# Optimization experiments

Hardware: AMD Instinct MI355X
Metric: run time of the kernel (lower is better)

## Reference

```python
import jax, jax.numpy as jnp
import numpy as np

N = 1048576        # batch
DTOT = 64          # total dims in u
D = 32             # transformed dims (len(nodes))
K = 40             # knots = num spline bins
B = 5.0            # tail bound: bins/2 = ceil(max|limit|)


def setup_inputs() -> dict:
    key = jax.random.key(0)
    k1, k2, k3, k4 = jax.random.split(key, 4)
    # scale inputs so they cover many bins and some fall in the identity tails
    u = jax.random.normal(k1, (N, DTOT), jnp.float32) * 3.0
    w = jax.random.uniform(k2, (D, K), jnp.float32, -0.5, 0.5)
    h = jax.random.uniform(k3, (D, K), jnp.float32, -0.5, 0.5)
    d = jax.random.uniform(k4, (D, K - 1), jnp.float32, -0.5, 0.5)
    nodes = jnp.arange(D, dtype=jnp.int32)
    return {"u": u, "w": w, "h": h, "d": d, "nodes": nodes}


def _rqs_forward(x, w, h, d):
    # x: [N, D] selected dims; w,h: [D, K]; d: [D, K-1]
    dt = x.dtype
    widths = jax.nn.softmax(w, axis=-1) * (2.0 * B)          # [D, K]
    cumw = jnp.concatenate(
        [jnp.full((D, 1), -B, dt), -B + jnp.cumsum(widths, -1)], -1)  # [D, K+1]
    heights = jax.nn.softmax(h, axis=-1) * (2.0 * B)
    cumh = jnp.concatenate(
        [jnp.full((D, 1), -B, dt), -B + jnp.cumsum(heights, -1)], -1)
    # interior derivatives via softplus, boundary derivatives fixed to 1 (linear tails)
    derivs = jnp.concatenate(
        [jnp.ones((D, 1), dt), jax.nn.softplus(d), jnp.ones((D, 1), dt)], -1)  # [D, K+1]

    inside = jnp.abs(x) <= B
    xc = jnp.clip(x, -B, B)
    # per-dim bin search (irregular, data-dependent)
    idx = jax.vmap(lambda kn, xd: jnp.searchsorted(kn, xd, side='right'))(cumw, xc.T).T - 1
    idx = jnp.clip(idx, 0, K - 1)                             # [N, D]

    dd = jnp.arange(D)[None, :]
    cw = cumw[dd, idx]; bw = widths[dd, idx]
    ch = cumh[dd, idx]; bh = heights[dd, idx]
    d0 = derivs[dd, idx]; d1 = derivs[dd, idx + 1]
    delta = bh / bw                                            # bin slope

    theta = (xc - cw) / bw
    t1m = theta * (1.0 - theta)
    denom = delta + (d0 + d1 - 2.0 * delta) * t1m
    num = bh * (delta * theta * theta + d0 * t1m)
    y = ch + num / denom
    logdet = (jnp.log(delta * delta * (d1 * theta * theta
                                       + 2.0 * delta * t1m
                                       + d0 * (1.0 - theta) ** 2))
              - 2.0 * jnp.log(denom))

    y = jnp.where(inside, y, x)                # identity tails
    logdet = jnp.where(inside, logdet, 0.0)
    return y, logdet.sum(-1)                   # [N, D], [N]


def reference(u, w, h, d, nodes):
    y, logd = _rqs_forward(u[:, nodes], w, h, d)
    x = u.at[:, nodes].set(y)
    return x, logd
```

## Files before the change

kernel.cpp:

```cpp
#include <hip/hip_runtime.h>
#include <math.h>

#define NROWS 1048576
#define DTOT  64
#define D     32
#define K     40
#define Bf    5.0f
#define G     128
#define GS    132
#define TP    (K + 1)

#define OFF_CUMW 0
#define OFF_DER  (D * (K + 1))
#define OFF_RBW  (2 * D * (K + 1))
#define OFF_CH   (2 * D * (K + 1) + D * K)
#define OFF_BH   (2 * D * (K + 1) + 2 * D * K)
#define OFF_GS_BYTES ((2 * D * (K + 1) + 3 * D * K) * 4)
#define WS_BYTES (OFF_GS_BYTES + D * G)

__global__ __launch_bounds__(64) void build_tables(
    const float* __restrict__ w, const float* __restrict__ h,
    const float* __restrict__ dk,
    float* __restrict__ cumw_g, float* __restrict__ der_g,
    float* __restrict__ rbw_g, float* __restrict__ ch_g,
    float* __restrict__ bh_g, unsigned char* __restrict__ gs_g)
{
    const int j = blockIdx.x;
    const int k = threadIdx.x;
    __shared__ float s_cumw[K + 1];

    float wv = (k < K) ? w[j * K + k] : -INFINITY;
    float hv = (k < K) ? h[j * K + k] : -INFINITY;
    float mw = wv, mh = hv;
    for (int m = 32; m > 0; m >>= 1) {
        mw = fmaxf(mw, __shfl_xor(mw, m));
        mh = fmaxf(mh, __shfl_xor(mh, m));
    }
    float ew = (k < K) ? __expf(wv - mw) : 0.f;
    float eh = (k < K) ? __expf(hv - mh) : 0.f;
    float sw = ew, sh = eh;
    for (int m = 32; m > 0; m >>= 1) {
        sw += __shfl_xor(sw, m);
        sh += __shfl_xor(sh, m);
    }
    float width  = ew / sw * (2.f * Bf);
    float height = eh / sh * (2.f * Bf);

    float iw = width, ih = height;
    for (int off = 1; off < 64; off <<= 1) {
        float a = __shfl_up(iw, off);
        float b = __shfl_up(ih, off);
        if (k >= off) { iw += a; ih += b; }
    }
    const float cw_k    = -Bf + (iw - width);
    const float ch_k    = -Bf + (ih - height);
    const float cw_next = -Bf + iw;

    if (k <= K) {
        float dv = 1.f;
        if (k > 0 && k < K) dv = log1pf(__expf(dk[j * (K - 1) + (k - 1)]));
        der_g[j * (K + 1) + k] = dv;
    }
    if (k < K) {
        cumw_g[j * (K + 1) + k] = cw_k;
        rbw_g[j * K + k] = 1.f / width;
        ch_g [j * K + k] = ch_k;
        bh_g [j * K + k] = height;
        s_cumw[k] = cw_k;
    }
    if (k == K - 1) {
        cumw_g[j * (K + 1) + K] = cw_next;
        s_cumw[K] = cw_next;
    }
    __syncthreads();

    for (int c = k; c < G; c += 64) {
        float L = -Bf + (2.f * Bf) * ((float)c / (float)G);
        int idx = 0;
        for (int m = 1; m < K; ++m)
            if (s_cumw[m] <= L) idx = m;
        gs_g[j * G + c] = (unsigned char)idx;
    }
}

__global__ __launch_bounds__(1024, 8) void rqs_main(
    const float4* __restrict__ u4,
    const float* __restrict__ cumw_g, const float* __restrict__ der_g,
    const float* __restrict__ rbw_g, const float* __restrict__ ch_g,
    const float* __restrict__ bh_g, const unsigned char* __restrict__ gs_g,
    float4* __restrict__ x4, float* __restrict__ logd, int ntiles)
{
    __shared__ float4 s_sel[D * TP];
    __shared__ float4 s_bin[D * TP];
    __shared__ unsigned char s_gs[D * GS];

    const int t = threadIdx.x;
    for (int e = t; e < D * K; e += 1024) {
        const int j = e / K, k = e - j * K;
        const float cw0 = cumw_g[j * (K + 1) + k];
        const float cw1 = cumw_g[j * (K + 1) + k + 1];
        const float rb0 = rbw_g[e];
        const float rb1 = (k < K - 1) ? rbw_g[e + 1] : 1.f;
        s_sel[j * TP + k] = make_float4(cw0, rb0, cw1, rb1);
        s_bin[j * TP + k] = make_float4(ch_g[e], bh_g[e],
                                        der_g[j * (K + 1) + k],
                                        der_g[j * (K + 1) + k + 1]);
    }
    for (int i = t; i < D * G / 4; i += 1024) {
        const int r = i >> 5, wi = i & 31;
        *(uint32_t*)(s_gs + r * GS + wi * 4) = ((const uint32_t*)gs_g)[i];
    }
    __syncthreads();

    const int seg = t & 7;
    const int rl  = t >> 3;

    int tile = blockIdx.x;
    float4 vt = make_float4(0.f, 0.f, 0.f, 0.f);
    float4 vp = make_float4(0.f, 0.f, 0.f, 0.f);
    if (tile < ntiles) {
        const int row = tile * 128 + rl;
        vt = u4[row * 16 + seg];
        vp = u4[row * 16 + 8 + seg];
    }

    for (; tile < ntiles; tile += gridDim.x) {
        const int next = tile + gridDim.x;
        float4 nt = make_float4(0.f, 0.f, 0.f, 0.f);
        float4 np = make_float4(0.f, 0.f, 0.f, 0.f);
        if (next < ntiles) {
            const int nrow = next * 128 + rl;
            nt = u4[nrow * 16 + seg];
            np = u4[nrow * 16 + 8 + seg];
        }

        const int row = tile * 128 + rl;
        x4[row * 16 + 8 + seg] = vp;

        float vv[4] = {vt.x, vt.y, vt.z, vt.w};
        float prod = 1.f;
#pragma unroll
        for (int c = 0; c < 4; ++c) {
            const int j = seg * 4 + c;
            const float x = vv[c];
            const bool inside = fabsf(x) <= Bf;
            const float xc = fminf(fmaxf(x, -Bf), Bf);

            int cell = (int)((xc + Bf) * (G / (2.f * Bf)));
            cell = min(cell, G - 1);
            int i = s_gs[j * GS + cell];

            const float4 s = s_sel[j * TP + i];
            const bool adv = (xc >= s.z) && (i < K - 1);
            const float cw  = adv ? s.z : s.x;
            const float rbw = adv ? s.w : s.y;
            i += adv;

            const float4 b = s_bin[j * TP + i];
            const float ch = b.x, bh = b.y, d0 = b.z, d1 = b.w;

            const float delta = bh * rbw;
            const float theta = (xc - cw) * rbw;
            const float omt   = 1.f - theta;
            const float t1m   = theta * omt;
            const float th2   = theta * theta;
            const float denom = fmaf(fmaf(-2.f, delta, d0 + d1), t1m, delta);
            const float num   = bh * fmaf(d0, t1m, delta * th2);
            const float rd    = __builtin_amdgcn_rcpf(denom);
            const float y     = fmaf(num, rd, ch);
            const float Ap    = fmaf(d1, th2,
                                 fmaf(2.f * delta, t1m, d0 * omt * omt));
            const float term  = delta * delta * Ap * (rd * rd);

            vv[c] = inside ? y : x;
            prod  = inside ? prod * term : prod;
        }
        x4[row * 16 + seg] = make_float4(vv[0], vv[1], vv[2], vv[3]);

        float ld = __logf(prod);
        ld += __shfl_xor(ld, 1);
        ld += __shfl_xor(ld, 2);
        ld += __shfl_xor(ld, 4);
        if (seg == 0) logd[row] = ld;

        vt = nt; vp = np;
    }
}

extern "C" void kernel_launch(void* const* d_in, const int* in_sizes, int n_in,
                              void* d_out, int out_size, void* d_ws, size_t ws_size,
                              hipStream_t stream) {
    const float* u  = (const float*)d_in[0];
    const float* w  = (const float*)d_in[1];
    const float* h  = (const float*)d_in[2];
    const float* dk = (const float*)d_in[3];

    float* ws   = (float*)d_ws;
    float* cumw = ws + OFF_CUMW;
    float* der  = ws + OFF_DER;
    float* rbw  = ws + OFF_RBW;
    float* ch   = ws + OFF_CH;
    float* bh   = ws + OFF_BH;
    unsigned char* gs = (unsigned char*)d_ws + OFF_GS_BYTES;

    float* xout = (float*)d_out;
    float* logd = (float*)d_out + (size_t)NROWS * DTOT;

    build_tables<<<D, 64, 0, stream>>>(w, h, dk, cumw, der, rbw, ch, bh, gs);

    const int ntiles = NROWS / 128;
    rqs_main<<<512, 1024, 0, stream>>>((const float4*)u, cumw, der, rbw, ch, bh,
                                       gs, (float4*)xout, logd, ntiles);
}
```

Baseline: 451.8 us.

## Use nontemporal stores, DPP reduction, and smaller blocks with a delayed passthrough load

Blocks shrink from 1024 to 512 threads and the grid grows from 512 to 768 blocks, so each tile now covers 64 rows. The passthrough half of each row is loaded in the current iteration instead of being prefetched, and both output halves plus logdet are written with nontemporal stores to reduce cache pollution. The 8-lane logdet reduction uses DPP row operations instead of shuffles. In exchange, loading the passthrough data late may expose its memory latency, and the DPP controls assume a fixed lane layout within each group of 8.

After: 465.8 us. 3.1% more time.

```diff
diff --git a/kernel.cpp b/kernel.cpp
--- a/kernel.cpp
+++ b/kernel.cpp
@@ -17,6 +17,18 @@
 #define OFF_BH   (2 * D * (K + 1) + 2 * D * K)
 #define OFF_GS_BYTES ((2 * D * (K + 1) + 3 * D * K) * 4)
 #define WS_BYTES (OFF_GS_BYTES + D * G)
+
+typedef float nt_f4 __attribute__((ext_vector_type(4)));
+
+__device__ __forceinline__ float dpp_add(float v, const int ctrl) {
+    int r;
+    switch (ctrl) {
+    case 0:  r = __builtin_amdgcn_update_dpp(0, __float_as_int(v), 0xB1,  0xF, 0xF, false); break;
+    case 1:  r = __builtin_amdgcn_update_dpp(0, __float_as_int(v), 0x4E,  0xF, 0xF, false); break;
+    default: r = __builtin_amdgcn_update_dpp(0, __float_as_int(v), 0x141, 0xF, 0xF, false); break;
+    }
+    return v + __int_as_float(r);
+}
 
 __global__ __launch_bounds__(64) void build_tables(
     const float* __restrict__ w, const float* __restrict__ h,
@@ -83,7 +95,7 @@
     }
 }
 
-__global__ __launch_bounds__(1024, 8) void rqs_main(
+__global__ __launch_bounds__(512, 6) void rqs_main(
     const float4* __restrict__ u4,
     const float* __restrict__ cumw_g, const float* __restrict__ der_g,
     const float* __restrict__ rbw_g, const float* __restrict__ ch_g,
@@ -95,7 +107,7 @@
     __shared__ unsigned char s_gs[D * GS];
 
     const int t = threadIdx.x;
-    for (int e = t; e < D * K; e += 1024) {
+    for (int e = t; e < D * K; e += 512) {
         const int j = e / K, k = e - j * K;
         const float cw0 = cumw_g[j * (K + 1) + k];
         const float cw1 = cumw_g[j * (K + 1) + k + 1];
@@ -106,7 +118,7 @@
                                         der_g[j * (K + 1) + k],
                                         der_g[j * (K + 1) + k + 1]);
     }
-    for (int i = t; i < D * G / 4; i += 1024) {
+    for (int i = t; i < D * G / 4; i += 512) {
         const int r = i >> 5, wi = i & 31;
         *(uint32_t*)(s_gs + r * GS + wi * 4) = ((const uint32_t*)gs_g)[i];
     }
@@ -117,25 +129,16 @@
 
     int tile = blockIdx.x;
     float4 vt = make_float4(0.f, 0.f, 0.f, 0.f);
-    float4 vp = make_float4(0.f, 0.f, 0.f, 0.f);
-    if (tile < ntiles) {
-        const int row = tile * 128 + rl;
-        vt = u4[row * 16 + seg];
-        vp = u4[row * 16 + 8 + seg];
-    }
+    if (tile < ntiles) vt = u4[(tile * 64 + rl) * 16 + seg];
 
     for (; tile < ntiles; tile += gridDim.x) {
+        const int row = tile * 64 + rl;
+
         const int next = tile + gridDim.x;
         float4 nt = make_float4(0.f, 0.f, 0.f, 0.f);
-        float4 np = make_float4(0.f, 0.f, 0.f, 0.f);
-        if (next < ntiles) {
-            const int nrow = next * 128 + rl;
-            nt = u4[nrow * 16 + seg];
-            np = u4[nrow * 16 + 8 + seg];
-        }
-
-        const int row = tile * 128 + rl;
-        x4[row * 16 + 8 + seg] = vp;
+        if (next < ntiles) nt = u4[(next * 64 + rl) * 16 + seg];
+
+        const float4 vp = u4[row * 16 + 8 + seg];
 
         float vv[4] = {vt.x, vt.y, vt.z, vt.w};
         float prod = 1.f;
@@ -175,15 +178,19 @@
             vv[c] = inside ? y : x;
             prod  = inside ? prod * term : prod;
         }
-        x4[row * 16 + seg] = make_float4(vv[0], vv[1], vv[2], vv[3]);
+        nt_f4 outv; outv.x = vv[0]; outv.y = vv[1]; outv.z = vv[2]; outv.w = vv[3];
+        __builtin_nontemporal_store(outv,
+            reinterpret_cast<nt_f4*>(&x4[row * 16 + seg]));
+        __builtin_nontemporal_store(*reinterpret_cast<const nt_f4*>(&vp),
+            reinterpret_cast<nt_f4*>(&x4[row * 16 + 8 + seg]));
 
         float ld = __logf(prod);
-        ld += __shfl_xor(ld, 1);
-        ld += __shfl_xor(ld, 2);
-        ld += __shfl_xor(ld, 4);
-        if (seg == 0) logd[row] = ld;
-
-        vt = nt; vp = np;
+        ld = dpp_add(ld, 0);
+        ld = dpp_add(ld, 1);
+        ld = dpp_add(ld, 2);
+        if (seg == 0) __builtin_nontemporal_store(ld, &logd[row]);
+
+        vt = nt;
     }
 }
 
@@ -208,7 +215,7 @@
 
     build_tables<<<D, 64, 0, stream>>>(w, h, dk, cumw, der, rbw, ch, bh, gs);
 
-    const int ntiles = NROWS / 128;
-    rqs_main<<<512, 1024, 0, stream>>>((const float4*)u, cumw, der, rbw, ch, bh,
-                                       gs, (float4*)xout, logd, ntiles);
-}
+    const int ntiles = NROWS / 64;
+    rqs_main<<<768, 512, 0, stream>>>((const float4*)u, cumw, der, rbw, ch, bh,
+                                      gs, (float4*)xout, logd, ntiles);
+}
```
